# Optimization experiments

Hardware: AMD Instinct MI355X
Metric: run time of the kernel (lower is better)

Reference implementation:

```python
import jax, jax.numpy as jnp
import numpy as np

D = 8
W = 256
CX = 63   # in_channels_xyz
CD = 27   # in_channels_dir
CF = 3    # in_channels_fea
SKIPS = (4,)
B = 262144


def _linear_init(k, fin, fout):
    # matches torch nn.Linear default: U(-1/sqrt(fin), 1/sqrt(fin))
    k1, k2 = jax.random.split(k)
    s = 1.0 / np.sqrt(fin)
    w = jax.random.uniform(k1, (fin, fout), jnp.float32, -s, s)
    b = jax.random.uniform(k2, (fout,), jnp.float32, -s, s)
    return w, b


def setup_inputs() -> dict:
    key = jax.random.key(0)
    ks = jax.random.split(key, 16)
    inp = {"x": jax.random.normal(ks[0], (B, CX + CD + CF), jnp.float32)}
    for i in range(D):
        fin = CX if i == 0 else (W + CX if i in SKIPS else W)
        w, b = _linear_init(ks[1 + i], fin, W)
        inp[f"w{i}"] = w
        inp[f"b{i}"] = b
    inp["wf"], inp["bf"] = _linear_init(ks[10], W, W)                 # xyz_encoding_final
    inp["wd"], inp["bd"] = _linear_init(ks[11], W + CD + CF, W // 2)  # dir_encoding
    inp["ws"], inp["bs"] = _linear_init(ks[12], W, 1)                 # sigma head
    inp["wr"], inp["br"] = _linear_init(ks[13], W // 2, 3)            # rgb head
    return inp


def reference(x, w0, b0, w1, b1, w2, b2, w3, b3, w4, b4, w5, b5, w6, b6, w7, b7,
              wf, bf, wd, bd, ws, bs, wr, br):
    layers = [(w0, b0), (w1, b1), (w2, b2), (w3, b3),
              (w4, b4), (w5, b5), (w6, b6), (w7, b7)]
    input_xyz = x[:, :CX]            # (B, 63)
    dir_fea = x[:, CX:]              # (B, 30) = dir(27) + feature(3)
    h = input_xyz
    for i, (w, b) in enumerate(layers):
        if i in SKIPS:
            h = jnp.concatenate([input_xyz, h], axis=-1)
        h = jax.nn.relu(h @ w + b)   # (B, 256)
    sigma = h @ ws + bs              # (B, 1)
    xyz_final = h @ wf + bf          # (B, 256), no activation
    d = jax.nn.relu(jnp.concatenate([xyz_final, dir_fea], axis=-1) @ wd + bd)  # (B, 128)
    rgb = jax.nn.sigmoid(d @ wr + br)  # (B, 3)
    return jnp.concatenate([rgb, sigma], axis=-1)  # (B, 4)
```

## Files before the change

### kernel.cpp

```cpp
#include <hip/hip_runtime.h>

typedef __bf16  bf16x8 __attribute__((ext_vector_type(8)));
typedef float   f32x4  __attribute__((ext_vector_type(4)));
typedef unsigned int uint32x2 __attribute__((ext_vector_type(2)));

#define MFMA16(a,b,c) __builtin_amdgcn_mfma_f32_16x16x32_bf16((a),(b),(c),0,0,0)

template<int V> struct ic_t { static constexpr int value = V; };

enum : int {
    OFF_W0 = 0,
    OFF_W1 = OFF_W0 + 256 * 64,
    OFF_W2 = OFF_W1 + 256 * 256,
    OFF_W3 = OFF_W2 + 256 * 256,
    OFF_W4 = OFF_W3 + 256 * 256,
    OFF_W5 = OFF_W4 + 256 * 320,
    OFF_W6 = OFF_W5 + 256 * 256,
    OFF_W7 = OFF_W6 + 256 * 256,
    OFF_WF = OFF_W7 + 256 * 256,
    OFF_WD = OFF_WF + 256 * 256,
    W_TOTAL = OFF_WD + 128 * 288
};

__device__ __forceinline__ unsigned short f2bf(float f) {
    unsigned int u = __float_as_uint(f);
    u += 0x7FFFu + ((u >> 16) & 1u);
    return (unsigned short)(u >> 16);
}

__device__ __forceinline__ void soft_barrier() {
    asm volatile("s_waitcnt lgkmcnt(0)" ::: "memory");
    __builtin_amdgcn_s_barrier();
}

__device__ __forceinline__ void prep_one(const float* __restrict__ src,
                                         unsigned short* __restrict__ dst,
                                         int fout, int Kp, int n1, int n2, int n3,
                                         int idx) {
    int n = idx / Kp;
    int k = idx - n * Kp;
    float v = 0.f;
    if (k < n1)                 v = src[k * fout + n];
    else if (k >= n2 && k < n3) v = src[(k - (n2 - n1)) * fout + n];
    dst[n * Kp + k] = f2bf(v);
}

__global__ void prep_kernel(const float* w0, const float* w1, const float* w2,
                            const float* w3, const float* w4, const float* w5,
                            const float* w6, const float* w7, const float* wf,
                            const float* wd, unsigned short* dst) {
    int i = blockIdx.x * 256 + threadIdx.x;
    if (i < 256 * 64)  { prep_one(w0, dst + OFF_W0, 256,  64,  63,  64,  64, i); return; }
    i -= 256 * 64;
    if (i < 256 * 256) { prep_one(w1, dst + OFF_W1, 256, 256, 256, 256, 256, i); return; }
    i -= 256 * 256;
    if (i < 256 * 256) { prep_one(w2, dst + OFF_W2, 256, 256, 256, 256, 256, i); return; }
    i -= 256 * 256;
    if (i < 256 * 256) { prep_one(w3, dst + OFF_W3, 256, 256, 256, 256, 256, i); return; }
    i -= 256 * 256;
    if (i < 256 * 320) { prep_one(w4, dst + OFF_W4, 256, 320,  63,  64, 320, i); return; }
    i -= 256 * 320;
    if (i < 256 * 256) { prep_one(w5, dst + OFF_W5, 256, 256, 256, 256, 256, i); return; }
    i -= 256 * 256;
    if (i < 256 * 256) { prep_one(w6, dst + OFF_W6, 256, 256, 256, 256, 256, i); return; }
    i -= 256 * 256;
    if (i < 256 * 256) { prep_one(w7, dst + OFF_W7, 256, 256, 256, 256, 256, i); return; }
    i -= 256 * 256;
    if (i < 256 * 256) { prep_one(wf, dst + OFF_WF, 256, 256, 256, 256, 256, i); return; }
    i -= 256 * 256;
    if (i < 128 * 288) { prep_one(wd, dst + OFF_WD, 128, 288, 286, 288, 288, i); return; }
}

struct Params {
    const float* x;
    const unsigned short* Wt;
    const float* b[8];
    const float* bfv;
    const float* bdv;
    const float* wsv;
    const float* bsv;
    const float* wrv;
    const float* brv;
    float* out;
};

__global__ __launch_bounds__(256, 2) void nerf_kernel(Params P) {
    __shared__ char Hs[32768];

    const int t    = threadIdx.x;
    const int lane = t & 63;
    const int wave = t >> 6;
    const int lr   = lane & 15;
    const int lk   = lane >> 4;
    const int blockRow = blockIdx.x << 6;

    bf16x8 bp0[4], bp1[4];
    {
        const unsigned short* Wb0 = P.Wt + OFF_W0 + (size_t)((wave << 6) + lr) * 64 + (lk << 3);
#pragma unroll
        for (int nt = 0; nt < 4; ++nt) {
            bp0[nt] = *(const bf16x8*)(Wb0 + (size_t)(nt << 4) * 64);
            bp1[nt] = *(const bf16x8*)(Wb0 + (size_t)(nt << 4) * 64 + 32);
        }
    }

    auto ldXg = [&](int mt, int c0, int lim) -> bf16x8 {
        const float* xr = P.x + (size_t)(blockRow + (mt << 4) + lr) * 93;
        bf16x8 r;
#pragma unroll
        for (int j = 0; j < 8; ++j) {
            int c = c0 + (lk << 3) + j;
            r[j] = (c < lim) ? (__bf16)xr[c] : (__bf16)0.f;
        }
        return r;
    };
    auto ldH = [&](int mt, int kt) -> bf16x8 {
        int row = (mt << 4) + lr;
        int off = (row * 512 + (kt << 6) + (lk << 4)) ^ ((row & 7) << 4);
        return *(const bf16x8*)(Hs + off);
    };

    auto gemm = [&](auto KTt, auto NTt, auto NTnt, auto&& getA,
                    const unsigned short* W, int Kp, const float* bias, bool dorelu,
                    const unsigned short* Wn, int Kpn, int cbn) {
        constexpr int KT  = decltype(KTt)::value;
        constexpr int NT  = decltype(NTt)::value;
        constexpr int NTn = decltype(NTnt)::value;
        const int colbase = wave * (NT << 4);
        const unsigned short* Wb = W + (size_t)(colbase + lr) * Kp + (lk << 3);
        const unsigned short* Wbn = (NTn > 0) ? Wn + (size_t)(cbn + lr) * Kpn + (lk << 3) : nullptr;

        f32x4 acc[4][NT];
        {
            f32x4 bfr[NT];
#pragma unroll
            for (int nt = 0; nt < NT; ++nt)
                bfr[nt] = *(const f32x4*)(bias + colbase + (nt << 4) + (lk << 2));
#pragma unroll
            for (int mt = 0; mt < 4; ++mt)
#pragma unroll
                for (int nt = 0; nt < NT; ++nt) acc[mt][nt] = bfr[nt];
        }

        bf16x8 aC[4], aN[4];
#pragma unroll
        for (int mt = 0; mt < 4; ++mt) { aC[mt] = getA(mt, 0); aN[mt] = aC[mt]; }

#pragma unroll
        for (int kt = 0; kt < KT; ++kt) {
            bf16x8 bp2[NT];
            if (kt + 2 < KT) {
#pragma unroll
                for (int nt = 0; nt < NT; ++nt)
                    bp2[nt] = *(const bf16x8*)(Wb + (size_t)(nt << 4) * Kp + ((kt + 2) << 5));
            } else if (NTn > 0) {
#pragma unroll
                for (int nt = 0; nt < (NTn > 0 ? NTn : 1); ++nt)
                    bp2[nt] = *(const bf16x8*)(Wbn + (size_t)(nt << 4) * Kpn + ((kt + 2 - KT) << 5));
            } else {
#pragma unroll
                for (int nt = 0; nt < NT; ++nt) bp2[nt] = bp1[nt];
            }
            if (kt + 1 < KT) {
#pragma unroll
                for (int mt = 0; mt < 4; ++mt) aN[mt] = getA(mt, kt + 1);
            }
            __builtin_amdgcn_s_setprio(1);
#pragma unroll
            for (int nt = 0; nt < NT; ++nt) {
#pragma unroll
                for (int mt = 0; mt < 4; ++mt)
                    acc[mt][nt] = MFMA16(bp0[nt], aC[mt], acc[mt][nt]);
            }
            __builtin_amdgcn_s_setprio(0);
#pragma unroll
            for (int nt = 0; nt < 4; ++nt) { bp0[nt] = bp1[nt]; }
#pragma unroll
            for (int nt = 0; nt < NT; ++nt) { bp1[nt] = bp2[nt]; }
#pragma unroll
            for (int mt = 0; mt < 4; ++mt) aC[mt] = aN[mt];
        }

        soft_barrier();

#pragma unroll
        for (int nt = 0; nt < NT; ++nt) {
#pragma unroll
            for (int mt = 0; mt < 4; ++mt) {
                f32x4 v = acc[mt][nt];
                if (dorelu) {
#pragma unroll
                    for (int e = 0; e < 4; ++e) v[e] = fmaxf(v[e], 0.f);
                }
                unsigned int lo, hi;
                asm("v_cvt_pk_bf16_f32 %0, %1, %2" : "=v"(lo) : "v"(v[0]), "v"(v[1]));
                asm("v_cvt_pk_bf16_f32 %0, %1, %2" : "=v"(hi) : "v"(v[2]), "v"(v[3]));
                int batch = (mt << 4) + lr;
                int off = (batch * 512 + ((colbase + (nt << 4) + (lk << 2)) << 1)) ^ ((batch & 7) << 4);
                uint32x2 w2 = {lo, hi};
                *(uint32x2*)(Hs + off) = w2;
            }
        }
    };

    const unsigned short* Wt = P.Wt;

    gemm(ic_t<2>{}, ic_t<4>{}, ic_t<4>{},
         [&](int mt, int kt) { return ldXg(mt, kt << 5, 63); },
         Wt + OFF_W0, 64, P.b[0], true, Wt + OFF_W1, 256, wave << 6);
    soft_barrier();

    {
        const unsigned short* Wc[3] = {Wt + OFF_W1, Wt + OFF_W2, Wt + OFF_W3};
        const unsigned short* Wn[3] = {Wt + OFF_W2, Wt + OFF_W3, Wt + OFF_W4};
        const int Kpn[3] = {256, 256, 320};
        const float* bc[3] = {P.b[1], P.b[2], P.b[3]};
        for (int i = 0; i < 3; ++i) {
            gemm(ic_t<8>{}, ic_t<4>{}, ic_t<4>{},
                 [&](int mt, int kt) { return ldH(mt, kt); },
                 Wc[i], 256, bc[i], true, Wn[i], Kpn[i], wave << 6);
            soft_barrier();
        }
    }

    gemm(ic_t<10>{}, ic_t<4>{}, ic_t<4>{},
         [&](int mt, int kt) { return (kt < 2) ? ldXg(mt, kt << 5, 63) : ldH(mt, kt - 2); },
         Wt + OFF_W4, 320, P.b[4], true, Wt + OFF_W5, 256, wave << 6);
    soft_barrier();

    {
        const unsigned short* Wc[3] = {Wt + OFF_W5, Wt + OFF_W6, Wt + OFF_W7};
        const unsigned short* Wn[3] = {Wt + OFF_W6, Wt + OFF_W7, Wt + OFF_WF};
        const float* bc[3] = {P.b[5], P.b[6], P.b[7]};
        for (int i = 0; i < 3; ++i) {
            gemm(ic_t<8>{}, ic_t<4>{}, ic_t<4>{},
                 [&](int mt, int kt) { return ldH(mt, kt); },
                 Wc[i], 256, bc[i], true, Wn[i], 256, wave << 6);
            soft_barrier();
        }
    }

    float sig;
    {
        int rr = t >> 2, q = t & 3;
        float sp = 0.f;
#pragma unroll
        for (int j = 0; j < 8; ++j) {
            int cb = (q << 6) + (j << 3);
            bf16x8 h8 = *(const bf16x8*)(Hs + ((rr * 512 + (cb << 1)) ^ ((rr & 7) << 4)));
#pragma unroll
            for (int e = 0; e < 8; ++e) sp += (float)h8[e] * P.wsv[cb + e];
        }
        sp += __shfl_xor(sp, 1);
        sp += __shfl_xor(sp, 2);
        sig = sp + P.bsv[0];
    }

    gemm(ic_t<8>{}, ic_t<4>{}, ic_t<2>{},
         [&](int mt, int kt) { return ldH(mt, kt); },
         Wt + OFF_WF, 256, P.bfv, false, Wt + OFF_WD, 288, wave << 5);
    soft_barrier();

    gemm(ic_t<9>{}, ic_t<2>{}, ic_t<0>{},
         [&](int mt, int kt) { return (kt < 8) ? ldH(mt, kt) : ldXg(mt, 63, 93); },
         Wt + OFF_WD, 288, P.bdv, true, nullptr, 0, 0);
    soft_barrier();

    {
        int rr = t >> 2, q = t & 3;
        float c0 = 0.f, c1 = 0.f, c2 = 0.f;
#pragma unroll
        for (int j = 0; j < 4; ++j) {
            int kb = (q << 5) + (j << 3);
            bf16x8 d8 = *(const bf16x8*)(Hs + ((rr * 512 + (kb << 1)) ^ ((rr & 7) << 4)));
#pragma unroll
            for (int e = 0; e < 8; ++e) {
                float dv = (float)d8[e];
                const float* w = P.wrv + (kb + e) * 3;
                c0 += dv * w[0]; c1 += dv * w[1]; c2 += dv * w[2];
            }
        }
        c0 += __shfl_xor(c0, 1); c0 += __shfl_xor(c0, 2);
        c1 += __shfl_xor(c1, 1); c1 += __shfl_xor(c1, 2);
        c2 += __shfl_xor(c2, 1); c2 += __shfl_xor(c2, 2);
        if (q == 0) {
            float4 o;
            o.x = 1.f / (1.f + __expf(-(c0 + P.brv[0])));
            o.y = 1.f / (1.f + __expf(-(c1 + P.brv[1])));
            o.z = 1.f / (1.f + __expf(-(c2 + P.brv[2])));
            o.w = sig;
            ((float4*)P.out)[blockRow + rr] = o;
        }
    }
}

extern "C" void kernel_launch(void* const* d_in, const int* in_sizes, int n_in,
                              void* d_out, int out_size, void* d_ws, size_t ws_size,
                              hipStream_t stream) {
    const float* x = (const float*)d_in[0];
    const float* w[8];
    const float* b[8];
    for (int i = 0; i < 8; ++i) {
        w[i] = (const float*)d_in[1 + 2 * i];
        b[i] = (const float*)d_in[2 + 2 * i];
    }
    const float* wf  = (const float*)d_in[17];
    const float* bfv = (const float*)d_in[18];
    const float* wd  = (const float*)d_in[19];
    const float* bdv = (const float*)d_in[20];
    const float* wsv = (const float*)d_in[21];
    const float* bsv = (const float*)d_in[22];
    const float* wrv = (const float*)d_in[23];
    const float* brv = (const float*)d_in[24];

    unsigned short* Wt = (unsigned short*)d_ws;

    prep_kernel<<<(W_TOTAL + 255) / 256, 256, 0, stream>>>(
        w[0], w[1], w[2], w[3], w[4], w[5], w[6], w[7], wf, wd, Wt);

    Params P;
    P.x = x; P.Wt = Wt;
    for (int i = 0; i < 8; ++i) P.b[i] = b[i];
    P.bfv = bfv; P.bdv = bdv; P.wsv = wsv; P.bsv = bsv; P.wrv = wrv; P.brv = brv;
    P.out = (float*)d_out;

    nerf_kernel<<<262144 / 64, 256, 0, stream>>>(P);
}
```

Before: 641.9 us.

## Switch to 32x32x16 MFMA tiles and double-buffer LDS activations

Replaces the 16x16x32 bf16 MFMA tiling with 32x32x16 MFMA, so each wave computes two 32-row tiles times two 32-column tiles. The fragment layouts, weight prefetch and epilogue store are rewritten to match. Activations now ping-pong between two 32KB LDS buffers, which removes the mid-gemm barrier before writeback. The cost is doubled LDS (64KB per block), which may limit the two-blocks-per-CU occupancy target, plus larger accumulator register pressure.

```diff
diff --git a/kernel.cpp b/kernel.cpp
--- a/kernel.cpp
+++ b/kernel.cpp
@@ -2,9 +2,10 @@
 
 typedef __bf16  bf16x8 __attribute__((ext_vector_type(8)));
 typedef float   f32x4  __attribute__((ext_vector_type(4)));
+typedef float   f32x16 __attribute__((ext_vector_type(16)));
 typedef unsigned int uint32x2 __attribute__((ext_vector_type(2)));
 
-#define MFMA16(a,b,c) __builtin_amdgcn_mfma_f32_16x16x32_bf16((a),(b),(c),0,0,0)
+#define MFMA32(a,b,c) __builtin_amdgcn_mfma_f32_32x32x16_bf16((a),(b),(c),0,0,0)
 
 template<int V> struct ic_t { static constexpr int value = V; };
 
@@ -85,129 +86,138 @@
 };
 
 __global__ __launch_bounds__(256, 2) void nerf_kernel(Params P) {
-    __shared__ char Hs[32768];
+    __shared__ char Hs0[32768];
+    __shared__ char Hs1[32768];
 
     const int t    = threadIdx.x;
     const int lane = t & 63;
     const int wave = t >> 6;
-    const int lr   = lane & 15;
-    const int lk   = lane >> 4;
+    const int l31  = lane & 31;
+    const int hi   = lane >> 5;
+    const int hi8  = hi << 3;
     const int blockRow = blockIdx.x << 6;
 
-    bf16x8 bp0[4], bp1[4];
-    {
-        const unsigned short* Wb0 = P.Wt + OFF_W0 + (size_t)((wave << 6) + lr) * 64 + (lk << 3);
-#pragma unroll
-        for (int nt = 0; nt < 4; ++nt) {
-            bp0[nt] = *(const bf16x8*)(Wb0 + (size_t)(nt << 4) * 64);
-            bp1[nt] = *(const bf16x8*)(Wb0 + (size_t)(nt << 4) * 64 + 32);
-        }
-    }
-
-    auto ldXg = [&](int mt, int c0, int lim) -> bf16x8 {
-        const float* xr = P.x + (size_t)(blockRow + (mt << 4) + lr) * 93;
+    bf16x8 aw0[2], aw1[2];
+    {
+        const unsigned short* Wb0 = P.Wt + OFF_W0 + (size_t)((wave << 6) + l31) * 64 + hi8;
+#pragma unroll
+        for (int ct = 0; ct < 2; ++ct) {
+            aw0[ct] = *(const bf16x8*)(Wb0 + (size_t)(ct << 5) * 64);
+            aw1[ct] = *(const bf16x8*)(Wb0 + (size_t)(ct << 5) * 64 + 16);
+        }
+    }
+
+    auto ldXg = [&](int rt, int c0, int lim) -> bf16x8 {
+        const float* xr = P.x + (size_t)(blockRow + (rt << 5) + l31) * 93;
         bf16x8 r;
 #pragma unroll
         for (int j = 0; j < 8; ++j) {
-            int c = c0 + (lk << 3) + j;
+            int c = c0 + hi8 + j;
             r[j] = (c < lim) ? (__bf16)xr[c] : (__bf16)0.f;
         }
         return r;
     };
-    auto ldH = [&](int mt, int kt) -> bf16x8 {
-        int row = (mt << 4) + lr;
-        int off = (row * 512 + (kt << 6) + (lk << 4)) ^ ((row & 7) << 4);
-        return *(const bf16x8*)(Hs + off);
+    auto ldH = [&](const char* B, int rt, int kt) -> bf16x8 {
+        int row = (rt << 5) + l31;
+        int off = (row * 512 + (kt << 5) + (hi << 4)) ^ ((row & 7) << 4);
+        return *(const bf16x8*)(B + off);
     };
 
-    auto gemm = [&](auto KTt, auto NTt, auto NTnt, auto&& getA,
+    auto gemm = [&](auto KTt, auto CTt, auto CTnt, auto&& getB,
                     const unsigned short* W, int Kp, const float* bias, bool dorelu,
-                    const unsigned short* Wn, int Kpn, int cbn) {
+                    char* dst, const unsigned short* Wn, int Kpn, int cbn) {
         constexpr int KT  = decltype(KTt)::value;
-        constexpr int NT  = decltype(NTt)::value;
-        constexpr int NTn = decltype(NTnt)::value;
-        const int colbase = wave * (NT << 4);
-        const unsigned short* Wb = W + (size_t)(colbase + lr) * Kp + (lk << 3);
-        const unsigned short* Wbn = (NTn > 0) ? Wn + (size_t)(cbn + lr) * Kpn + (lk << 3) : nullptr;
-
-        f32x4 acc[4][NT];
-        {
-            f32x4 bfr[NT];
-#pragma unroll
-            for (int nt = 0; nt < NT; ++nt)
-                bfr[nt] = *(const f32x4*)(bias + colbase + (nt << 4) + (lk << 2));
-#pragma unroll
-            for (int mt = 0; mt < 4; ++mt)
-#pragma unroll
-                for (int nt = 0; nt < NT; ++nt) acc[mt][nt] = bfr[nt];
-        }
-
-        bf16x8 aC[4], aN[4];
-#pragma unroll
-        for (int mt = 0; mt < 4; ++mt) { aC[mt] = getA(mt, 0); aN[mt] = aC[mt]; }
+        constexpr int CT  = decltype(CTt)::value;
+        constexpr int CTn = decltype(CTnt)::value;
+        const int cb = wave * (CT << 5);
+        const unsigned short* Wb = W + (size_t)(cb + l31) * Kp + hi8;
+        const unsigned short* Wbn = (CTn > 0) ? Wn + (size_t)(cbn + l31) * Kpn + hi8 : nullptr;
+
+        f32x16 acc[2][CT];
+#pragma unroll
+        for (int ct = 0; ct < CT; ++ct) {
+            f32x16 ini;
+#pragma unroll
+            for (int q = 0; q < 4; ++q) {
+                f32x4 bq = *(const f32x4*)(bias + cb + (ct << 5) + (q << 3) + (hi << 2));
+#pragma unroll
+                for (int e = 0; e < 4; ++e) ini[(q << 2) + e] = bq[e];
+            }
+            acc[0][ct] = ini;
+            acc[1][ct] = ini;
+        }
+
+        bf16x8 bC[2], bN[2];
+#pragma unroll
+        for (int rt = 0; rt < 2; ++rt) { bC[rt] = getB(rt, 0); bN[rt] = bC[rt]; }
 
 #pragma unroll
         for (int kt = 0; kt < KT; ++kt) {
-            bf16x8 bp2[NT];
+            bf16x8 awN[2];
             if (kt + 2 < KT) {
 #pragma unroll
-                for (int nt = 0; nt < NT; ++nt)
-                    bp2[nt] = *(const bf16x8*)(Wb + (size_t)(nt << 4) * Kp + ((kt + 2) << 5));
-            } else if (NTn > 0) {
-#pragma unroll
-                for (int nt = 0; nt < (NTn > 0 ? NTn : 1); ++nt)
-                    bp2[nt] = *(const bf16x8*)(Wbn + (size_t)(nt << 4) * Kpn + ((kt + 2 - KT) << 5));
+                for (int ct = 0; ct < CT; ++ct)
+                    awN[ct] = *(const bf16x8*)(Wb + (size_t)(ct << 5) * Kp + ((kt + 2) << 4));
+            } else if (CTn > 0) {
+#pragma unroll
+                for (int ct = 0; ct < (CTn > 0 ? CTn : 1); ++ct)
+                    awN[ct] = *(const bf16x8*)(Wbn + (size_t)(ct << 5) * Kpn + ((kt + 2 - KT) << 4));
             } else {
 #pragma unroll
-                for (int nt = 0; nt < NT; ++nt) bp2[nt] = bp1[nt];
+                for (int ct = 0; ct < 2; ++ct) awN[ct] = aw1[ct];
             }
             if (kt + 1 < KT) {
 #pragma unroll
-                for (int mt = 0; mt < 4; ++mt) aN[mt] = getA(mt, kt + 1);
+                for (int rt = 0; rt < 2; ++rt) bN[rt] = getB(rt, kt + 1);
             }
             __builtin_amdgcn_s_setprio(1);
 #pragma unroll
-            for (int nt = 0; nt < NT; ++nt) {
-#pragma unroll
-                for (int mt = 0; mt < 4; ++mt)
-                    acc[mt][nt] = MFMA16(bp0[nt], aC[mt], acc[mt][nt]);
+            for (int ct = 0; ct < CT; ++ct) {
+                acc[0][ct] = MFMA32(aw0[ct], bC[0], acc[0][ct]);
+                acc[1][ct] = MFMA32(aw0[ct], bC[1], acc[1][ct]);
             }
             __builtin_amdgcn_s_setprio(0);
 #pragma unroll
-            for (int nt = 0; nt < 4; ++nt) { bp0[nt] = bp1[nt]; }
-#pragma unroll
-            for (int nt = 0; nt < NT; ++nt) { bp1[nt] = bp2[nt]; }
-#pragma unroll
-            for (int mt = 0; mt < 4; ++mt) aC[mt] = aN[mt];
-        }
-
-        soft_barrier();
-
-#pragma unroll
-        for (int nt = 0; nt < NT; ++nt) {
-#pragma unroll
-            for (int mt = 0; mt < 4; ++mt) {
-                f32x4 v = acc[mt][nt];
-                if (dorelu) {
-#pragma unroll
-                    for (int e = 0; e < 4; ++e) v[e] = fmaxf(v[e], 0.f);
+            for (int ct = 0; ct < 2; ++ct) { aw0[ct] = aw1[ct]; aw1[ct] = awN[ct]; }
+#pragma unroll
+            for (int rt = 0; rt < 2; ++rt) bC[rt] = bN[rt];
+        }
+
+#pragma unroll
+        for (int ct = 0; ct < CT; ++ct) {
+#pragma unroll
+            for (int rt = 0; rt < 2; ++rt) {
+                int row = (rt << 5) + l31;
+                int rsw = (row & 7) << 4;
+#pragma unroll
+                for (int q = 0; q < 4; ++q) {
+                    float v0 = acc[rt][ct][(q << 2) + 0];
+                    float v1 = acc[rt][ct][(q << 2) + 1];
+                    float v2 = acc[rt][ct][(q << 2) + 2];
+                    float v3 = acc[rt][ct][(q << 2) + 3];
+                    if (dorelu) {
+                        v0 = fmaxf(v0, 0.f); v1 = fmaxf(v1, 0.f);
+                        v2 = fmaxf(v2, 0.f); v3 = fmaxf(v3, 0.f);
+                    }
+                    unsigned int lo, hi2;
+                    asm("v_cvt_pk_bf16_f32 %0, %1, %2" : "=v"(lo)  : "v"(v0), "v"(v1));
+                    asm("v_cvt_pk_bf16_f32 %0, %1, %2" : "=v"(hi2) : "v"(v2), "v"(v3));
+                    int col = cb + (ct << 5) + (q << 3) + (hi << 2);
+                    int off = (row * 512 + (col << 1)) ^ rsw;
+                    uint32x2 w2 = {lo, hi2};
+                    *(uint32x2*)(dst + off) = w2;
                 }
-                unsigned int lo, hi;
-                asm("v_cvt_pk_bf16_f32 %0, %1, %2" : "=v"(lo) : "v"(v[0]), "v"(v[1]));
-                asm("v_cvt_pk_bf16_f32 %0, %1, %2" : "=v"(hi) : "v"(v[2]), "v"(v[3]));
-                int batch = (mt << 4) + lr;
-                int off = (batch * 512 + ((colbase + (nt << 4) + (lk << 2)) << 1)) ^ ((batch & 7) << 4);
-                uint32x2 w2 = {lo, hi};
-                *(uint32x2*)(Hs + off) = w2;
             }
         }
     };
 
     const unsigned short* Wt = P.Wt;
-
-    gemm(ic_t<2>{}, ic_t<4>{}, ic_t<4>{},
-         [&](int mt, int kt) { return ldXg(mt, kt << 5, 63); },
-         Wt + OFF_W0, 64, P.b[0], true, Wt + OFF_W1, 256, wave << 6);
+    char* cur = Hs0;
+    char* alt = Hs1;
+
+    gemm(ic_t<4>{}, ic_t<2>{}, ic_t<2>{},
+         [&](int rt, int kt) { return ldXg(rt, kt << 4, 63); },
+         Wt + OFF_W0, 64, P.b[0], true, cur, Wt + OFF_W1, 256, wave << 6);
     soft_barrier();
 
     {
@@ -216,27 +226,30 @@
         const int Kpn[3] = {256, 256, 320};
         const float* bc[3] = {P.b[1], P.b[2], P.b[3]};
         for (int i = 0; i < 3; ++i) {
-            gemm(ic_t<8>{}, ic_t<4>{}, ic_t<4>{},
-                 [&](int mt, int kt) { return ldH(mt, kt); },
-                 Wc[i], 256, bc[i], true, Wn[i], Kpn[i], wave << 6);
+            gemm(ic_t<16>{}, ic_t<2>{}, ic_t<2>{},
+                 [&](int rt, int kt) { return ldH(cur, rt, kt); },
+                 Wc[i], 256, bc[i], true, alt, Wn[i], Kpn[i], wave << 6);
             soft_barrier();
-        }
-    }
-
-    gemm(ic_t<10>{}, ic_t<4>{}, ic_t<4>{},
-         [&](int mt, int kt) { return (kt < 2) ? ldXg(mt, kt << 5, 63) : ldH(mt, kt - 2); },
-         Wt + OFF_W4, 320, P.b[4], true, Wt + OFF_W5, 256, wave << 6);
+            char* tmp = cur; cur = alt; alt = tmp;
+        }
+    }
+
+    gemm(ic_t<20>{}, ic_t<2>{}, ic_t<2>{},
+         [&](int rt, int kt) { return (kt < 4) ? ldXg(rt, kt << 4, 63) : ldH(cur, rt, kt - 4); },
+         Wt + OFF_W4, 320, P.b[4], true, alt, Wt + OFF_W5, 256, wave << 6);
     soft_barrier();
+    { char* tmp = cur; cur = alt; alt = tmp; }
 
     {
         const unsigned short* Wc[3] = {Wt + OFF_W5, Wt + OFF_W6, Wt + OFF_W7};
         const unsigned short* Wn[3] = {Wt + OFF_W6, Wt + OFF_W7, Wt + OFF_WF};
         const float* bc[3] = {P.b[5], P.b[6], P.b[7]};
         for (int i = 0; i < 3; ++i) {
-            gemm(ic_t<8>{}, ic_t<4>{}, ic_t<4>{},
-                 [&](int mt, int kt) { return ldH(mt, kt); },
-                 Wc[i], 256, bc[i], true, Wn[i], 256, wave << 6);
+            gemm(ic_t<16>{}, ic_t<2>{}, ic_t<2>{},
+                 [&](int rt, int kt) { return ldH(cur, rt, kt); },
+                 Wc[i], 256, bc[i], true, alt, Wn[i], 256, wave << 6);
             soft_barrier();
+            char* tmp = cur; cur = alt; alt = tmp;
         }
     }
 
@@ -246,24 +259,27 @@
         float sp = 0.f;
 #pragma unroll
         for (int j = 0; j < 8; ++j) {
-            int cb = (q << 6) + (j << 3);
-            bf16x8 h8 = *(const bf16x8*)(Hs + ((rr * 512 + (cb << 1)) ^ ((rr & 7) << 4)));
-#pragma unroll
-            for (int e = 0; e < 8; ++e) sp += (float)h8[e] * P.wsv[cb + e];
+            int cb2 = (q << 6) + (j << 3);
+            bf16x8 h8 = *(const bf16x8*)(cur + ((rr * 512 + (cb2 << 1)) ^ ((rr & 7) << 4)));
+#pragma unroll
+            for (int e = 0; e < 8; ++e) sp += (float)h8[e] * P.wsv[cb2 + e];
         }
         sp += __shfl_xor(sp, 1);
         sp += __shfl_xor(sp, 2);
         sig = sp + P.bsv[0];
     }
 
-    gemm(ic_t<8>{}, ic_t<4>{}, ic_t<2>{},
-         [&](int mt, int kt) { return ldH(mt, kt); },
-         Wt + OFF_WF, 256, P.bfv, false, Wt + OFF_WD, 288, wave << 5);
+    gemm(ic_t<16>{}, ic_t<2>{}, ic_t<1>{},
+         [&](int rt, int kt) { return ldH(cur, rt, kt); },
+         Wt + OFF_WF, 256, P.bfv, false, alt, Wt + OFF_WD, 288, wave << 5);
     soft_barrier();
-
-    gemm(ic_t<9>{}, ic_t<2>{}, ic_t<0>{},
-         [&](int mt, int kt) { return (kt < 8) ? ldH(mt, kt) : ldXg(mt, 63, 93); },
-         Wt + OFF_WD, 288, P.bdv, true, nullptr, 0, 0);
+    { char* tmp = cur; cur = alt; alt = tmp; }
+
+    gemm(ic_t<18>{}, ic_t<1>{}, ic_t<0>{},
+         [&](int rt, int kt) {
+             return (kt < 16) ? ldH(cur, rt, kt) : ldXg(rt, 63 + ((kt - 16) << 4), 93);
+         },
+         Wt + OFF_WD, 288, P.bdv, true, alt, nullptr, 0, 0);
     soft_barrier();
 
     {
@@ -272,7 +288,7 @@
 #pragma unroll
         for (int j = 0; j < 4; ++j) {
             int kb = (q << 5) + (j << 3);
-            bf16x8 d8 = *(const bf16x8*)(Hs + ((rr * 512 + (kb << 1)) ^ ((rr & 7) << 4)));
+            bf16x8 d8 = *(const bf16x8*)(alt + ((rr * 512 + (kb << 1)) ^ ((rr & 7) << 4)));
 #pragma unroll
             for (int e = 0; e < 8; ++e) {
                 float dv = (float)d8[e];
```

Result: slower. 668.6 us (+4.1%).

## Loop over layers with double-buffered LDS activations and runtime layer tables

Applied to the files above, without the earlier changes.

Replaces the fully unrolled, template-specialized per-layer GEMM calls with a runtime loop over nine layers. Layer parameters come from constant tables and a device-side bias pointer table written by the prep kernel. Activations ping-pong between two 32KB LDS halves, which removes the pre-epilogue barrier in each layer, and the xyz_final output is kept in a separate buffer for the dir layer. This cuts code size and the number of barriers, but doubles LDS to 64KB per block, which may limit occupancy. It also swaps the cross-layer weight prefetch and compile-time unrolling for runtime-indexed loads.

```diff
diff --git a/kernel.cpp b/kernel.cpp
--- a/kernel.cpp
+++ b/kernel.cpp
@@ -5,8 +5,6 @@
 typedef unsigned int uint32x2 __attribute__((ext_vector_type(2)));
 
 #define MFMA16(a,b,c) __builtin_amdgcn_mfma_f32_16x16x32_bf16((a),(b),(c),0,0,0)
-
-template<int V> struct ic_t { static constexpr int value = V; };
 
 enum : int {
     OFF_W0 = 0,
@@ -22,6 +20,11 @@
     W_TOTAL = OFF_WD + 128 * 288
 };
 
+__constant__ int cWOff[9] = {OFF_W0, OFF_W1, OFF_W2, OFF_W3, OFF_W4, OFF_W5, OFF_W6, OFF_W7, OFF_WF};
+__constant__ int cKp[9]   = {64, 256, 256, 256, 320, 256, 256, 256, 256};
+__constant__ int cKT[9]   = {2, 8, 8, 8, 10, 8, 8, 8, 8};
+__constant__ int cXKt[9]  = {2, 0, 0, 0, 2, 0, 0, 0, 0};
+
 __device__ __forceinline__ unsigned short f2bf(float f) {
     unsigned int u = __float_as_uint(f);
     u += 0x7FFFu + ((u >> 16) & 1u);
@@ -48,7 +51,15 @@
 __global__ void prep_kernel(const float* w0, const float* w1, const float* w2,
                             const float* w3, const float* w4, const float* w5,
                             const float* w6, const float* w7, const float* wf,
-                            const float* wd, unsigned short* dst) {
+                            const float* wd,
+                            const float* b0, const float* b1, const float* b2,
+                            const float* b3, const float* b4, const float* b5,
+                            const float* b6, const float* b7, const float* bfv,
+                            unsigned short* dst, const float** tbl) {
+    if (blockIdx.x == 0 && threadIdx.x == 0) {
+        tbl[0] = b0; tbl[1] = b1; tbl[2] = b2; tbl[3] = b3; tbl[4] = b4;
+        tbl[5] = b5; tbl[6] = b6; tbl[7] = b7; tbl[8] = bfv;
+    }
     int i = blockIdx.x * 256 + threadIdx.x;
     if (i < 256 * 64)  { prep_one(w0, dst + OFF_W0, 256,  64,  63,  64,  64, i); return; }
     i -= 256 * 64;
@@ -74,8 +85,7 @@
 struct Params {
     const float* x;
     const unsigned short* Wt;
-    const float* b[8];
-    const float* bfv;
+    const float* const* bias9;
     const float* bdv;
     const float* wsv;
     const float* bsv;
@@ -85,106 +95,133 @@
 };
 
 __global__ __launch_bounds__(256, 2) void nerf_kernel(Params P) {
-    __shared__ char Hs[32768];
+    __shared__ char Hs[65536];
 
     const int t    = threadIdx.x;
     const int lane = t & 63;
     const int wave = t >> 6;
     const int lr   = lane & 15;
     const int lk   = lane >> 4;
+    const int lkb  = lk << 4;
     const int blockRow = blockIdx.x << 6;
 
-    bf16x8 bp0[4], bp1[4];
-    {
-        const unsigned short* Wb0 = P.Wt + OFF_W0 + (size_t)((wave << 6) + lr) * 64 + (lk << 3);
-#pragma unroll
-        for (int nt = 0; nt < 4; ++nt) {
-            bp0[nt] = *(const bf16x8*)(Wb0 + (size_t)(nt << 4) * 64);
-            bp1[nt] = *(const bf16x8*)(Wb0 + (size_t)(nt << 4) * 64 + 32);
-        }
-    }
-
-    auto ldXg = [&](int mt, int c0, int lim) -> bf16x8 {
-        const float* xr = P.x + (size_t)(blockRow + (mt << 4) + lr) * 93;
+    int rowOff[4], swz[4];
+    const float* xr[4];
+#pragma unroll
+    for (int mt = 0; mt < 4; ++mt) {
+        int row = (mt << 4) + lr;
+        rowOff[mt] = row * 512;
+        swz[mt]    = (row & 7) << 4;
+        xr[mt]     = P.x + (size_t)(blockRow + row) * 93;
+    }
+
+    auto ldXfrag = [&](const float* xrm, int kt) -> bf16x8 {
+        int c0 = (kt << 5) + (lk << 3);
         bf16x8 r;
 #pragma unroll
         for (int j = 0; j < 8; ++j) {
-            int c = c0 + (lk << 3) + j;
-            r[j] = (c < lim) ? (__bf16)xr[c] : (__bf16)0.f;
+            int c = c0 + j;
+            r[j] = (c < 63) ? (__bf16)xrm[c] : (__bf16)0.f;
         }
         return r;
     };
-    auto ldH = [&](int mt, int kt) -> bf16x8 {
-        int row = (mt << 4) + lr;
-        int off = (row * 512 + (kt << 6) + (lk << 4)) ^ ((row & 7) << 4);
-        return *(const bf16x8*)(Hs + off);
+    auto ldHfrag = [&](const char* buf, int mt, int kt) -> bf16x8 {
+        int col = (kt << 6) + lkb;
+        return *(const bf16x8*)(buf + rowOff[mt] + (col ^ swz[mt]));
     };
 
-    auto gemm = [&](auto KTt, auto NTt, auto NTnt, auto&& getA,
-                    const unsigned short* W, int Kp, const float* bias, bool dorelu,
-                    const unsigned short* Wn, int Kpn, int cbn) {
-        constexpr int KT  = decltype(KTt)::value;
-        constexpr int NT  = decltype(NTt)::value;
-        constexpr int NTn = decltype(NTnt)::value;
-        const int colbase = wave * (NT << 4);
-        const unsigned short* Wb = W + (size_t)(colbase + lr) * Kp + (lk << 3);
-        const unsigned short* Wbn = (NTn > 0) ? Wn + (size_t)(cbn + lr) * Kpn + (lk << 3) : nullptr;
-
-        f32x4 acc[4][NT];
-        {
-            f32x4 bfr[NT];
-#pragma unroll
-            for (int nt = 0; nt < NT; ++nt)
-                bfr[nt] = *(const f32x4*)(bias + colbase + (nt << 4) + (lk << 2));
-#pragma unroll
-            for (int mt = 0; mt < 4; ++mt)
-#pragma unroll
-                for (int nt = 0; nt < NT; ++nt) acc[mt][nt] = bfr[nt];
-        }
-
-        bf16x8 aC[4], aN[4];
-#pragma unroll
-        for (int mt = 0; mt < 4; ++mt) { aC[mt] = getA(mt, 0); aN[mt] = aC[mt]; }
-
-#pragma unroll
-        for (int kt = 0; kt < KT; ++kt) {
-            bf16x8 bp2[NT];
-            if (kt + 2 < KT) {
-#pragma unroll
-                for (int nt = 0; nt < NT; ++nt)
-                    bp2[nt] = *(const bf16x8*)(Wb + (size_t)(nt << 4) * Kp + ((kt + 2) << 5));
-            } else if (NTn > 0) {
-#pragma unroll
-                for (int nt = 0; nt < (NTn > 0 ? NTn : 1); ++nt)
-                    bp2[nt] = *(const bf16x8*)(Wbn + (size_t)(nt << 4) * Kpn + ((kt + 2 - KT) << 5));
-            } else {
-#pragma unroll
-                for (int nt = 0; nt < NT; ++nt) bp2[nt] = bp1[nt];
-            }
-            if (kt + 1 < KT) {
-#pragma unroll
-                for (int mt = 0; mt < 4; ++mt) aN[mt] = getA(mt, kt + 1);
-            }
+#pragma unroll 1
+    for (int L = 0; L < 9; ++L) {
+        const int Kp  = cKp[L];
+        const int KT  = cKT[L];
+        const int xKt = cXKt[L];
+        const unsigned short* W = P.Wt + cWOff[L];
+        const float* bias = P.bias9[L];
+        const char* rb = Hs + (((L & 1) ^ 1) << 15);
+        char* wb = Hs + ((L & 1) << 15);
+        const int cb = wave << 6;
+
+        int voff[4];
+#pragma unroll
+        for (int nt = 0; nt < 4; ++nt)
+            voff[nt] = (cb + (nt << 4) + lr) * Kp + (lk << 3);
+
+        f32x4 acc[4][4];
+#pragma unroll
+        for (int nt = 0; nt < 4; ++nt) {
+            f32x4 bv = *(const f32x4*)(bias + cb + (nt << 4) + (lk << 2));
+#pragma unroll
+            for (int mt = 0; mt < 4; ++mt) acc[mt][nt] = bv;
+        }
+
+        bf16x8 aE[4], aO[4], bE[4], bO[4];
+        if (0 < xKt) {
+#pragma unroll
+            for (int mt = 0; mt < 4; ++mt) aE[mt] = ldXfrag(xr[mt], 0);
+        } else {
+#pragma unroll
+            for (int mt = 0; mt < 4; ++mt) aE[mt] = ldHfrag(rb, mt, 0);
+        }
+        if (1 < xKt) {
+#pragma unroll
+            for (int mt = 0; mt < 4; ++mt) aO[mt] = ldXfrag(xr[mt], 1);
+        } else {
+#pragma unroll
+            for (int mt = 0; mt < 4; ++mt) aO[mt] = ldHfrag(rb, mt, 1 - xKt);
+        }
+#pragma unroll
+        for (int nt = 0; nt < 4; ++nt) {
+            bE[nt] = *(const bf16x8*)(W + voff[nt]);
+            bO[nt] = *(const bf16x8*)(W + voff[nt] + 32);
+        }
+
+#pragma unroll 1
+        for (int kt = 0; kt < KT; kt += 2) {
             __builtin_amdgcn_s_setprio(1);
 #pragma unroll
-            for (int nt = 0; nt < NT; ++nt) {
+            for (int nt = 0; nt < 4; ++nt)
 #pragma unroll
                 for (int mt = 0; mt < 4; ++mt)
-                    acc[mt][nt] = MFMA16(bp0[nt], aC[mt], acc[mt][nt]);
-            }
+                    acc[mt][nt] = MFMA16(bE[nt], aE[mt], acc[mt][nt]);
             __builtin_amdgcn_s_setprio(0);
-#pragma unroll
-            for (int nt = 0; nt < 4; ++nt) { bp0[nt] = bp1[nt]; }
-#pragma unroll
-            for (int nt = 0; nt < NT; ++nt) { bp1[nt] = bp2[nt]; }
-#pragma unroll
-            for (int mt = 0; mt < 4; ++mt) aC[mt] = aN[mt];
-        }
-
-        soft_barrier();
-
-#pragma unroll
-        for (int nt = 0; nt < NT; ++nt) {
+            {
+                int kE = (kt + 2 < KT) ? kt + 2 : KT - 1;
+                if (kE < xKt) {
+#pragma unroll
+                    for (int mt = 0; mt < 4; ++mt) aE[mt] = ldXfrag(xr[mt], kE);
+                } else {
+#pragma unroll
+                    for (int mt = 0; mt < 4; ++mt) aE[mt] = ldHfrag(rb, mt, kE - xKt);
+                }
+#pragma unroll
+                for (int nt = 0; nt < 4; ++nt)
+                    bE[nt] = *(const bf16x8*)(W + voff[nt] + (kE << 5));
+            }
+            __builtin_amdgcn_s_setprio(1);
+#pragma unroll
+            for (int nt = 0; nt < 4; ++nt)
+#pragma unroll
+                for (int mt = 0; mt < 4; ++mt)
+                    acc[mt][nt] = MFMA16(bO[nt], aO[mt], acc[mt][nt]);
+            __builtin_amdgcn_s_setprio(0);
+            {
+                int kO = (kt + 3 < KT) ? kt + 3 : KT - 1;
+                if (kO < xKt) {
+#pragma unroll
+                    for (int mt = 0; mt < 4; ++mt) aO[mt] = ldXfrag(xr[mt], kO);
+                } else {
+#pragma unroll
+                    for (int mt = 0; mt < 4; ++mt) aO[mt] = ldHfrag(rb, mt, kO - xKt);
+                }
+#pragma unroll
+                for (int nt = 0; nt < 4; ++nt)
+                    bO[nt] = *(const bf16x8*)(W + voff[nt] + (kO << 5));
+            }
+        }
+
+        const bool dorelu = (L < 8);
+#pragma unroll
+        for (int nt = 0; nt < 4; ++nt) {
 #pragma unroll
             for (int mt = 0; mt < 4; ++mt) {
                 f32x4 v = acc[mt][nt];
@@ -195,50 +232,16 @@
                 unsigned int lo, hi;
                 asm("v_cvt_pk_bf16_f32 %0, %1, %2" : "=v"(lo) : "v"(v[0]), "v"(v[1]));
                 asm("v_cvt_pk_bf16_f32 %0, %1, %2" : "=v"(hi) : "v"(v[2]), "v"(v[3]));
-                int batch = (mt << 4) + lr;
-                int off = (batch * 512 + ((colbase + (nt << 4) + (lk << 2)) << 1)) ^ ((batch & 7) << 4);
+                int colb = (cb + (nt << 4) + (lk << 2)) << 1;
+                int off = rowOff[mt] + (colb ^ swz[mt]);
                 uint32x2 w2 = {lo, hi};
-                *(uint32x2*)(Hs + off) = w2;
-            }
-        }
-    };
-
-    const unsigned short* Wt = P.Wt;
-
-    gemm(ic_t<2>{}, ic_t<4>{}, ic_t<4>{},
-         [&](int mt, int kt) { return ldXg(mt, kt << 5, 63); },
-         Wt + OFF_W0, 64, P.b[0], true, Wt + OFF_W1, 256, wave << 6);
-    soft_barrier();
-
-    {
-        const unsigned short* Wc[3] = {Wt + OFF_W1, Wt + OFF_W2, Wt + OFF_W3};
-        const unsigned short* Wn[3] = {Wt + OFF_W2, Wt + OFF_W3, Wt + OFF_W4};
-        const int Kpn[3] = {256, 256, 320};
-        const float* bc[3] = {P.b[1], P.b[2], P.b[3]};
-        for (int i = 0; i < 3; ++i) {
-            gemm(ic_t<8>{}, ic_t<4>{}, ic_t<4>{},
-                 [&](int mt, int kt) { return ldH(mt, kt); },
-                 Wc[i], 256, bc[i], true, Wn[i], Kpn[i], wave << 6);
-            soft_barrier();
-        }
-    }
-
-    gemm(ic_t<10>{}, ic_t<4>{}, ic_t<4>{},
-         [&](int mt, int kt) { return (kt < 2) ? ldXg(mt, kt << 5, 63) : ldH(mt, kt - 2); },
-         Wt + OFF_W4, 320, P.b[4], true, Wt + OFF_W5, 256, wave << 6);
-    soft_barrier();
-
-    {
-        const unsigned short* Wc[3] = {Wt + OFF_W5, Wt + OFF_W6, Wt + OFF_W7};
-        const unsigned short* Wn[3] = {Wt + OFF_W6, Wt + OFF_W7, Wt + OFF_WF};
-        const float* bc[3] = {P.b[5], P.b[6], P.b[7]};
-        for (int i = 0; i < 3; ++i) {
-            gemm(ic_t<8>{}, ic_t<4>{}, ic_t<4>{},
-                 [&](int mt, int kt) { return ldH(mt, kt); },
-                 Wc[i], 256, bc[i], true, Wn[i], 256, wave << 6);
-            soft_barrier();
-        }
-    }
+                *(uint32x2*)(wb + off) = w2;
+            }
+        }
+        soft_barrier();
+    }
+    char* HsXF = Hs;
+    char* HsH  = Hs + 32768;
 
     float sig;
     {
@@ -246,25 +249,117 @@
         float sp = 0.f;
 #pragma unroll
         for (int j = 0; j < 8; ++j) {
-            int cb = (q << 6) + (j << 3);
-            bf16x8 h8 = *(const bf16x8*)(Hs + ((rr * 512 + (cb << 1)) ^ ((rr & 7) << 4)));
-#pragma unroll
-            for (int e = 0; e < 8; ++e) sp += (float)h8[e] * P.wsv[cb + e];
+            int cb2 = (q << 6) + (j << 3);
+            bf16x8 h8 = *(const bf16x8*)(HsH + ((rr * 512 + (cb2 << 1)) ^ ((rr & 7) << 4)));
+#pragma unroll
+            for (int e = 0; e < 8; ++e) sp += (float)h8[e] * P.wsv[cb2 + e];
         }
         sp += __shfl_xor(sp, 1);
         sp += __shfl_xor(sp, 2);
         sig = sp + P.bsv[0];
     }
-
-    gemm(ic_t<8>{}, ic_t<4>{}, ic_t<2>{},
-         [&](int mt, int kt) { return ldH(mt, kt); },
-         Wt + OFF_WF, 256, P.bfv, false, Wt + OFF_WD, 288, wave << 5);
     soft_barrier();
 
-    gemm(ic_t<9>{}, ic_t<2>{}, ic_t<0>{},
-         [&](int mt, int kt) { return (kt < 8) ? ldH(mt, kt) : ldXg(mt, 63, 93); },
-         Wt + OFF_WD, 288, P.bdv, true, nullptr, 0, 0);
-    soft_barrier();
+    {
+        const unsigned short* W = P.Wt + OFF_WD;
+        const int cb = wave << 5;
+        int voff[2];
+#pragma unroll
+        for (int nt = 0; nt < 2; ++nt)
+            voff[nt] = (cb + (nt << 4) + lr) * 288 + (lk << 3);
+
+        f32x4 acc[4][2];
+#pragma unroll
+        for (int nt = 0; nt < 2; ++nt) {
+            f32x4 bv = *(const f32x4*)(P.bdv + cb + (nt << 4) + (lk << 2));
+#pragma unroll
+            for (int mt = 0; mt < 4; ++mt) acc[mt][nt] = bv;
+        }
+
+        auto ldDir = [&](const float* xrm) -> bf16x8 {
+            int c0 = 63 + (lk << 3);
+            bf16x8 r;
+#pragma unroll
+            for (int j = 0; j < 8; ++j) {
+                int c = c0 + j;
+                r[j] = (c < 93) ? (__bf16)xrm[c] : (__bf16)0.f;
+            }
+            return r;
+        };
+
+        bf16x8 aE[4], aO[4], bE[2], bO[2];
+#pragma unroll
+        for (int mt = 0; mt < 4; ++mt) { aE[mt] = ldHfrag(HsXF, mt, 0); aO[mt] = ldHfrag(HsXF, mt, 1); }
+#pragma unroll
+        for (int nt = 0; nt < 2; ++nt) {
+            bE[nt] = *(const bf16x8*)(W + voff[nt]);
+            bO[nt] = *(const bf16x8*)(W + voff[nt] + 32);
+        }
+
+#pragma unroll 1
+        for (int kt = 0; kt < 8; kt += 2) {
+            __builtin_amdgcn_s_setprio(1);
+#pragma unroll
+            for (int nt = 0; nt < 2; ++nt)
+#pragma unroll
+                for (int mt = 0; mt < 4; ++mt)
+                    acc[mt][nt] = MFMA16(bE[nt], aE[mt], acc[mt][nt]);
+            __builtin_amdgcn_s_setprio(0);
+            {
+                int kE = kt + 2;
+                if (kE == 8) {
+#pragma unroll
+                    for (int mt = 0; mt < 4; ++mt) aE[mt] = ldDir(xr[mt]);
+                } else {
+#pragma unroll
+                    for (int mt = 0; mt < 4; ++mt) aE[mt] = ldHfrag(HsXF, mt, kE);
+                }
+#pragma unroll
+                for (int nt = 0; nt < 2; ++nt)
+                    bE[nt] = *(const bf16x8*)(W + voff[nt] + (kE << 5));
+            }
+            __builtin_amdgcn_s_setprio(1);
+#pragma unroll
+            for (int nt = 0; nt < 2; ++nt)
+#pragma unroll
+                for (int mt = 0; mt < 4; ++mt)
+                    acc[mt][nt] = MFMA16(bO[nt], aO[mt], acc[mt][nt]);
+            __builtin_amdgcn_s_setprio(0);
+            {
+                int kO = (kt + 3 < 8) ? kt + 3 : 7;
+#pragma unroll
+                for (int mt = 0; mt < 4; ++mt) aO[mt] = ldHfrag(HsXF, mt, kO);
+#pragma unroll
+                for (int nt = 0; nt < 2; ++nt)
+                    bO[nt] = *(const bf16x8*)(W + voff[nt] + (kO << 5));
+            }
+        }
+        __builtin_amdgcn_s_setprio(1);
+#pragma unroll
+        for (int nt = 0; nt < 2; ++nt)
+#pragma unroll
+            for (int mt = 0; mt < 4; ++mt)
+                acc[mt][nt] = MFMA16(bE[nt], aE[mt], acc[mt][nt]);
+        __builtin_amdgcn_s_setprio(0);
+
+#pragma unroll
+        for (int nt = 0; nt < 2; ++nt) {
+#pragma unroll
+            for (int mt = 0; mt < 4; ++mt) {
+                f32x4 v = acc[mt][nt];
+#pragma unroll
+                for (int e = 0; e < 4; ++e) v[e] = fmaxf(v[e], 0.f);
+                unsigned int lo, hi;
+                asm("v_cvt_pk_bf16_f32 %0, %1, %2" : "=v"(lo) : "v"(v[0]), "v"(v[1]));
+                asm("v_cvt_pk_bf16_f32 %0, %1, %2" : "=v"(hi) : "v"(v[2]), "v"(v[3]));
+                int colb = (cb + (nt << 4) + (lk << 2)) << 1;
+                int off = rowOff[mt] + (colb ^ swz[mt]);
+                uint32x2 w2 = {lo, hi};
+                *(uint32x2*)(HsH + off) = w2;
+            }
+        }
+        soft_barrier();
+    }
 
     {
         int rr = t >> 2, q = t & 3;
@@ -272,7 +367,7 @@
 #pragma unroll
         for (int j = 0; j < 4; ++j) {
             int kb = (q << 5) + (j << 3);
-            bf16x8 d8 = *(const bf16x8*)(Hs + ((rr * 512 + (kb << 1)) ^ ((rr & 7) << 4)));
+            bf16x8 d8 = *(const bf16x8*)(HsH + ((rr * 512 + (kb << 1)) ^ ((rr & 7) << 4)));
 #pragma unroll
             for (int e = 0; e < 8; ++e) {
                 float dv = (float)d8[e];
@@ -314,14 +409,16 @@
     const float* brv = (const float*)d_in[24];
 
     unsigned short* Wt = (unsigned short*)d_ws;
+    const float** tbl = (const float**)((char*)d_ws + (size_t)W_TOTAL * 2);
 
     prep_kernel<<<(W_TOTAL + 255) / 256, 256, 0, stream>>>(
-        w[0], w[1], w[2], w[3], w[4], w[5], w[6], w[7], wf, wd, Wt);
+        w[0], w[1], w[2], w[3], w[4], w[5], w[6], w[7], wf, wd,
+        b[0], b[1], b[2], b[3], b[4], b[5], b[6], b[7], bfv,
+        Wt, tbl);
 
     Params P;
-    P.x = x; P.Wt = Wt;
-    for (int i = 0; i < 8; ++i) P.b[i] = b[i];
-    P.bfv = bfv; P.bdv = bdv; P.wsv = wsv; P.bsv = bsv; P.wrv = wrv; P.brv = brv;
+    P.x = x; P.Wt = Wt; P.bias9 = tbl;
+    P.bdv = bdv; P.wsv = wsv; P.bsv = bsv; P.wrv = wrv; P.brv = brv;
     P.out = (float*)d_out;
 
     nerf_kernel<<<262144 / 64, 256, 0, stream>>>(P);
```

After: 784.8 us. 1.22x slower.
